# Kernel tuning notes

Measured on AMD Instinct MI355X. Metric: run time of the kernel, lower is better.

The kernel has to match this reference:

```python
import jax, jax.numpy as jnp
import numpy as np

DIM = 256
HEADS = 8
HD = DIM // HEADS  # 32
RPE_H = 512
STRIDE = 16
B, NQ = 4, 300
HH, WW = 64, 64
N = HH * WW


def setup_inputs() -> dict:
    key = jax.random.key(0)
    ks = jax.random.split(key, 24)

    def lin(k, fan_in, fan_out):
        return (jax.random.normal(k, (fan_in, fan_out), jnp.float32)
                / np.float32(np.sqrt(fan_in)))

    # boxes in absolute pixel coords (image is WW*STRIDE = 1024 px wide)
    rp_xy = jax.random.uniform(ks[0], (B, NQ, 1, 2), jnp.float32) * (WW * STRIDE)
    rp_wh = jax.random.uniform(ks[1], (B, NQ, 1, 2), jnp.float32) * 256.0 + 16.0
    reference_points = jnp.concatenate([rp_xy, rp_wh], axis=-1)  # [B,NQ,1,4]

    inp = {
        "query": jax.random.normal(ks[2], (B, NQ, DIM), jnp.float32),
        "reference_points": reference_points,
        "k_input_flatten": jax.random.normal(ks[3], (B, N, DIM), jnp.float32),
        "v_input_flatten": jax.random.normal(ks[4], (B, N, DIM), jnp.float32),
        "input_spatial_shapes": jnp.array([[HH, WW]], dtype=jnp.int32),
        "input_padding_mask": (jax.random.uniform(ks[5], (B, N)) < 0.1).astype(jnp.int32),
        # projections (stored as [in, out]; y = x @ W + b)
        "Wq": lin(ks[6], DIM, DIM), "bq": jnp.zeros((DIM,), jnp.float32),
        "Wk": lin(ks[7], DIM, DIM), "bk": jnp.zeros((DIM,), jnp.float32),
        "Wv": lin(ks[8], DIM, DIM), "bv": jnp.zeros((DIM,), jnp.float32),
        "Wp": lin(ks[9], DIM, DIM), "bp": jnp.zeros((DIM,), jnp.float32),
        # CPB MLP 1 (x-deltas): Linear(2,512)+ReLU+Linear(512,HEADS,no bias)
        "W1x": lin(ks[10], 2, RPE_H), "b1x": jnp.zeros((RPE_H,), jnp.float32),
        "W2x": lin(ks[11], RPE_H, HEADS),
        # CPB MLP 2 (y-deltas)
        "W1y": lin(ks[12], 2, RPE_H), "b1y": jnp.zeros((RPE_H,), jnp.float32),
        "W2y": lin(ks[13], RPE_H, HEADS),
    }
    return inp


def reference(query, reference_points, k_input_flatten, v_input_flatten,
              input_spatial_shapes, input_padding_mask,
              Wq, bq, Wk, bk, Wv, bv, Wp, bp,
              W1x, b1x, W2x, W1y, b1y, W2y):
    h = int(input_spatial_shapes[0, 0])
    w = int(input_spatial_shapes[0, 1])
    scale = HD ** -0.5

    # cxcywh -> (x1,y1,x2,y2)
    c, s = reference_points[..., :2], reference_points[..., 2:]
    ref_pts = jnp.concatenate([c - s / 2, c + s / 2], axis=-1)  # [B,NQ,1,4]

    pos_x = (jnp.arange(w, dtype=jnp.float32) + 0.5) * STRIDE  # [w]
    pos_y = (jnp.arange(h, dtype=jnp.float32) + 0.5) * STRIDE  # [h]
    delta_x = ref_pts[..., 0::2] - pos_x[None, None, :, None]  # [B,NQ,w,2]
    delta_y = ref_pts[..., 1::2] - pos_y[None, None, :, None]  # [B,NQ,h,2]

    rpe_x = jax.nn.relu(delta_x @ W1x + b1x) @ W2x  # [B,NQ,w,HEADS]
    rpe_y = jax.nn.relu(delta_y @ W1y + b1y) @ W2y  # [B,NQ,h,HEADS]
    rpe = rpe_x[:, :, None, :, :] + rpe_y[:, :, :, None, :]  # [B,NQ,h,w,H]

    Bq, Nq, C = query.shape
    rpe = rpe.reshape(Bq, Nq, h * w, HEADS).transpose(0, 3, 1, 2)  # [B,H,NQ,N]

    q = (query @ Wq + bq).reshape(Bq, Nq, HEADS, HD).transpose(0, 2, 1, 3) * scale
    k = (k_input_flatten @ Wk + bk).reshape(Bq, -1, HEADS, HD).transpose(0, 2, 1, 3)
    v = (v_input_flatten @ Wv + bv).reshape(Bq, -1, HEADS, HD).transpose(0, 2, 1, 3)

    attn = jnp.einsum('bhqd,bhkd->bhqk', q, k) + rpe
    attn = attn + input_padding_mask[:, None, None, :].astype(attn.dtype) * (-100.0)
    fi = jnp.finfo(attn.dtype)
    attn = jnp.clip(attn, fi.min, fi.max)
    attn = jax.nn.softmax(attn, axis=-1)

    x = jnp.einsum('bhqk,bhkd->bhqd', attn, v)
    x = x.transpose(0, 2, 1, 3).reshape(Bq, Nq, C)
    return x @ Wp + bp
```

## Files before the change

### kernel.cpp

```cpp
#include <hip/hip_runtime.h>
#include <math.h>

#define B_   4
#define NQ_  300
#define DIM_ 256
#define H_   8
#define HD_  32
#define N_   4096

typedef _Float16 f16;
typedef f16   f16x8 __attribute__((ext_vector_type(8)));
typedef f16   f16x4 __attribute__((ext_vector_type(4)));
typedef float f32x4 __attribute__((ext_vector_type(4)));

__global__ __launch_bounds__(256) void prep_wt(
    const float* __restrict__ Wq, const float* __restrict__ Wk,
    const float* __restrict__ Wv, const float* __restrict__ Wp,
    f16* __restrict__ WT, float qscale)
{
  __shared__ float t[64][65];
  const int z = blockIdx.z;
  const float* W = z == 0 ? Wq : z == 1 ? Wk : z == 2 ? Wv : Wp;
  const float s = z == 0 ? qscale : 1.0f;
  f16* O = WT + (size_t)z * 65536;
  const int k0 = blockIdx.y * 64, n0 = blockIdx.x * 64;
  const int r = threadIdx.x >> 2, c0 = (threadIdx.x & 3) * 16;
#pragma unroll
  for (int c = 0; c < 16; c += 4) {
    float4 v = *(const float4*)(W + (size_t)(k0 + r) * 256 + n0 + c0 + c);
    t[r][c0 + c] = v.x; t[r][c0 + c + 1] = v.y;
    t[r][c0 + c + 2] = v.z; t[r][c0 + c + 3] = v.w;
  }
  __syncthreads();
  f16* orow = O + (size_t)(n0 + r) * 256 + k0 + c0;
#pragma unroll
  for (int c = 0; c < 16; c += 4) {
    f16x4 p;
    p[0] = (f16)(t[c0 + c + 0][r] * s);
    p[1] = (f16)(t[c0 + c + 1][r] * s);
    p[2] = (f16)(t[c0 + c + 2][r] * s);
    p[3] = (f16)(t[c0 + c + 3][r] * s);
    *(f16x4*)(orow + c) = p;
  }
}

__device__ __forceinline__ void gemm_body(
    const void* __restrict__ Ain, const f16* __restrict__ WT,
    const float* __restrict__ bias, void* __restrict__ C,
    int M, float scale, int a_f16, int mode, int bm, int bn, int tid)
{
  __shared__ f16 As[64][40];
  __shared__ f16 Bs[64][40];
  const int lane = tid & 63;
  const int wv = tid >> 6;
  const int l15 = lane & 15, g = lane >> 4;
  const int arow = tid >> 2, akq = (tid & 3) * 8;

  f32x4 acc[4];
#pragma unroll
  for (int nt = 0; nt < 4; ++nt) acc[nt] = (f32x4){0.f, 0.f, 0.f, 0.f};

  for (int k0 = 0; k0 < 256; k0 += 32) {
    {
      const int gm = bm + arow;
      f16x8 av;
      if (gm < M) {
        if (a_f16 == 2) {
          const int bb2 = gm / NQ_, qq2 = gm % NQ_;
          const int kk = k0 + akq;
          av = *(const f16x8*)((const f16*)Ain +
              (((size_t)(bb2 * H_ + (kk >> 5)) * NQ_) + qq2) * 32 + (kk & 31));
        } else if (a_f16 == 1) {
          av = *(const f16x8*)((const f16*)Ain + (size_t)gm * 256 + k0 + akq);
        } else {
          const float* ap = (const float*)Ain + (size_t)gm * 256 + k0 + akq;
          float4 a0 = *(const float4*)ap;
          float4 a1 = *(const float4*)(ap + 4);
          av[0] = (f16)a0.x; av[1] = (f16)a0.y; av[2] = (f16)a0.z; av[3] = (f16)a0.w;
          av[4] = (f16)a1.x; av[5] = (f16)a1.y; av[6] = (f16)a1.z; av[7] = (f16)a1.w;
        }
      } else {
#pragma unroll
        for (int i = 0; i < 8; ++i) av[i] = (f16)0.f;
      }
      *(f16x8*)&As[arow][akq] = av;
      *(f16x8*)&Bs[arow][akq] =
          *(const f16x8*)(WT + (size_t)(bn + arow) * 256 + k0 + akq);
    }
    __syncthreads();
    const f16x8 af = *(const f16x8*)&As[wv * 16 + l15][g * 8];
#pragma unroll
    for (int nt = 0; nt < 4; ++nt) {
      const f16x8 bf = *(const f16x8*)&Bs[nt * 16 + l15][g * 8];
      acc[nt] = __builtin_amdgcn_mfma_f32_16x16x32_f16(af, bf, acc[nt], 0, 0, 0);
    }
    __syncthreads();
  }

#pragma unroll
  for (int nt = 0; nt < 4; ++nt) {
    const int n = bn + nt * 16 + l15;
    const float bv = bias[n] * scale;
    if (mode == 2) {
      const int m0 = bm + wv * 16 + g * 4;
      const int bb = m0 >> 12, nk = m0 & 4095;
      f16x4 pk;
#pragma unroll
      for (int r = 0; r < 4; ++r) pk[r] = (f16)(acc[nt][r] + bv);
      *(f16x4*)((f16*)C + (size_t)bb * (256 * 4096) + (size_t)n * 4096 + nk) = pk;
    } else {
#pragma unroll
      for (int r = 0; r < 4; ++r) {
        const int m = bm + wv * 16 + g * 4 + r;
        if (m >= M) continue;
        const float v = acc[nt][r] + bv;
        if (mode == 0)      ((float*)C)[(size_t)m * 256 + n] = v;
        else if (mode == 1) ((f16*)C)[(size_t)m * 256 + n] = (f16)v;
        else                ((f16*)C)[((((size_t)(m >> 12)) * H_ + (n >> 5)) * N_
                                       + (m & 4095)) * 32 + (n & 31)] = (f16)v;
      }
    }
  }
}

__global__ __launch_bounds__(256) void proj_qkv(
    const float* __restrict__ query, const float* __restrict__ kin,
    const float* __restrict__ vin, const f16* __restrict__ WT,
    const float* __restrict__ bq, const float* __restrict__ bk,
    const float* __restrict__ bv, f16* __restrict__ Qf,
    f16* __restrict__ Kf, f16* __restrict__ Vtf, float qscale)
{
  const int z = blockIdx.z;
  const int bm = blockIdx.y * 64, bn = blockIdx.x * 64;
  if (z == 0) {
    if (bm >= B_ * NQ_) return;
    gemm_body(query, WT, bq, Qf, B_ * NQ_, qscale, 0, 1, bm, bn, threadIdx.x);
  } else if (z == 1) {
    gemm_body(kin, WT + 65536, bk, Kf, B_ * N_, 1.0f, 0, 3, bm, bn, threadIdx.x);
  } else {
    gemm_body(vin, WT + 2 * 65536, bv, Vtf, B_ * N_, 1.0f, 0, 2, bm, bn, threadIdx.x);
  }
}

__global__ __launch_bounds__(256) void gemm_out(
    const f16* __restrict__ X, const f16* __restrict__ WT,
    const float* __restrict__ bp, float* __restrict__ out)
{
  gemm_body(X, WT + 3 * 65536, bp, out, B_ * NQ_, 1.0f, 2, 0,
            blockIdx.y * 64, blockIdx.x * 64, threadIdx.x);
}

__global__ __launch_bounds__(256) void rpe_kernel(
    const float* __restrict__ refpts,
    const float* __restrict__ W1x, const float* __restrict__ b1x, const float* __restrict__ W2x,
    const float* __restrict__ W1y, const float* __restrict__ b1y, const float* __restrict__ W2y,
    float* __restrict__ rpx, float* __restrict__ rpy)
{
  __shared__ float sRed[4][64][9];
  const int tid = threadIdx.x;
  const int lane = tid & 63;
  const int wv = __builtin_amdgcn_readfirstlane(tid >> 6);
  const int bq = blockIdx.x;
  const int axis = blockIdx.y;
  const float* W1 = axis ? W1y : W1x;
  const float* b1 = axis ? b1y : b1x;
  const float* W2 = axis ? W2y : W2x;
  float* out = axis ? rpy : rpx;

  const float c  = refpts[bq * 4 + axis];
  const float sz = refpts[bq * 4 + 2 + axis];
  const float pos = (lane + 0.5f) * 16.0f;
  const float d0 = c - 0.5f * sz - pos;
  const float d1 = c + 0.5f * sz - pos;
  float acc[8] = {};
  const int r0 = wv * 128;
#pragma unroll 4
  for (int i = 0; i < 128; ++i) {
    const int r = r0 + i;
    const float w10 = W1[r], w11 = W1[512 + r], bb = b1[r];
    const float hv = fmaxf(fmaf(d0, w10, fmaf(d1, w11, bb)), 0.0f);
    const float* w2r = W2 + r * 8;
#pragma unroll
    for (int hh = 0; hh < 8; ++hh) acc[hh] += hv * w2r[hh];
  }
#pragma unroll
  for (int hh = 0; hh < 8; ++hh) sRed[wv][lane][hh] = acc[hh];
  __syncthreads();
  for (int idx = tid; idx < 512; idx += 256) {
    const int hh = idx >> 6, jj = idx & 63;
    out[(size_t)bq * 512 + idx] =
        sRed[0][jj][hh] + sRed[1][jj][hh] + sRed[2][jj][hh] + sRed[3][jj][hh];
  }
}

__global__ __launch_bounds__(512, 4) void attn_mfma(
    const f16* __restrict__ Qf, const f16* __restrict__ Kf,
    const f16* __restrict__ Vtf, const float* __restrict__ rpx,
    const float* __restrict__ rpy, const int* __restrict__ mask,
    f16* __restrict__ X)
{
  __shared__ float smask[N_];
  __shared__ float srx[16][68];
  __shared__ float sry[16][68];
  __shared__ float mO[7][8][64];
  __shared__ float mlm[7][16];
  __shared__ float mll[7][16];

  const int tid = threadIdx.x;
  const int lane = tid & 63;
  const int kh = tid >> 6;
  const int bid = blockIdx.x;
  const int lg  = (bid & 7) * 80 + (bid >> 3);
  const int qg = lg % 20;
  const int h  = (lg / 20) % H_;
  const int b  = lg / (20 * H_);
  const int q0 = qg * 16;
  const float L2E = 1.44269504f;

  {
    const int4* mm4 = (const int4*)(mask + b * N_);
    for (int i = tid; i < N_ / 4; i += 512) {
      int4 mm = mm4[i];
      smask[4 * i + 0] = -100.f * L2E * (float)mm.x;
      smask[4 * i + 1] = -100.f * L2E * (float)mm.y;
      smask[4 * i + 2] = -100.f * L2E * (float)mm.z;
      smask[4 * i + 3] = -100.f * L2E * (float)mm.w;
    }
  }
  for (int i = tid; i < 1024; i += 512) {
    int qq = i >> 6, j = i & 63;
    int qg2 = q0 + qq; if (qg2 > NQ_ - 1) qg2 = NQ_ - 1;
    size_t base = (size_t)(b * NQ_ + qg2) * 512 + (size_t)h * 64 + j;
    srx[qq][j] = rpx[base] * L2E;
    sry[qq][j] = rpy[base] * L2E;
  }
  __syncthreads();

  const int l15 = lane & 15, g = lane >> 4;
  const int qrow0 = q0 + l15;
  const int qa = qrow0 > NQ_ - 1 ? NQ_ - 1 : qrow0;

  const f16x8 qf0 = *(const f16x8*)(Qf + (size_t)(b * NQ_ + qa) * 256 + h * 32 + g * 8);

  f32x4 O00 = {0.f,0.f,0.f,0.f}, O01 = {0.f,0.f,0.f,0.f};
  float lacc0 = 0.f;
  float mrun0 = -1e30f;
  const f16* kb  = Kf + (size_t)(b * H_ + h) * N_ * 32 + g * 8;
  const f16* v0p = Vtf + (size_t)(b * 256 + h * 32 + l15) * N_ + g * 4;
  const f16* v1p = v0p + (size_t)16 * N_;

  for (int sp = 0; sp < 8; ++sp) {
    const int kbase = kh * 512 + sp * 64;
    f16x8 kf[4];
    f16x4 va[4], vb[4];
#pragma unroll
    for (int cc = 0; cc < 4; ++cc) {
      kf[cc] = *(const f16x8*)(kb + (size_t)(kbase + cc * 16 + l15) * 32);
      va[cc] = *(const f16x4*)(v0p + kbase + cc * 16);
      vb[cc] = *(const f16x4*)(v1p + kbase + cc * 16);
    }
    f32x4 s0[4];
    float lm0 = -1e30f;
#pragma unroll
    for (int cc = 0; cc < 4; ++cc) {
      const int k0 = kbase + cc * 16;
      f32x4 S0 = __builtin_amdgcn_mfma_f32_16x16x32_f16(
          kf[cc], qf0, (f32x4){0.f,0.f,0.f,0.f}, 0, 0, 0);
      const float ry0 = sry[l15][k0 >> 6];
      const float4 rx0 = *(const float4*)&srx[l15][(k0 & 63) + g * 4];
      const float4 sm = *(const float4*)&smask[k0 + g * 4];
      s0[cc][0] = fmaf(S0[0], L2E, rx0.x + sm.x + ry0);
      s0[cc][1] = fmaf(S0[1], L2E, rx0.y + sm.y + ry0);
      s0[cc][2] = fmaf(S0[2], L2E, rx0.z + sm.z + ry0);
      s0[cc][3] = fmaf(S0[3], L2E, rx0.w + sm.w + ry0);
      lm0 = fmaxf(lm0, fmaxf(fmaxf(s0[cc][0], s0[cc][1]), fmaxf(s0[cc][2], s0[cc][3])));
    }
    lm0 = fmaxf(lm0, __shfl_xor(lm0, 16));
    lm0 = fmaxf(lm0, __shfl_xor(lm0, 32));
    const float mn0 = fmaxf(mrun0, lm0);
    const float f0 = exp2f(mrun0 - mn0);
    mrun0 = mn0;
    lacc0 *= f0;
#pragma unroll
    for (int r = 0; r < 4; ++r) { O00[r] *= f0; O01[r] *= f0; }
#pragma unroll
    for (int cc = 0; cc < 4; ++cc) {
      f16x4 pf0;
#pragma unroll
      for (int r = 0; r < 4; ++r) {
        const float p0 = exp2f(s0[cc][r] - mrun0);
        lacc0 += p0;
        pf0[r] = (f16)p0;
      }
      O00 = __builtin_amdgcn_mfma_f32_16x16x16f16(va[cc], pf0, O00, 0, 0, 0);
      O01 = __builtin_amdgcn_mfma_f32_16x16x16f16(vb[cc], pf0, O01, 0, 0, 0);
    }
  }

  lacc0 += __shfl_xor(lacc0, 16); lacc0 += __shfl_xor(lacc0, 32);

  if (kh > 0) {
#pragma unroll
    for (int r = 0; r < 4; ++r) {
      mO[kh - 1][r][lane]     = O00[r];
      mO[kh - 1][4 + r][lane] = O01[r];
    }
    if (lane < 16) {
      mlm[kh - 1][lane] = mrun0;
      mll[kh - 1][lane] = lacc0;
    }
  }
  __syncthreads();
  if (kh == 0) {
    float ms = mrun0;
#pragma unroll
    for (int w = 0; w < 7; ++w) ms = fmaxf(ms, mlm[w][l15]);
    const float fme = exp2f(mrun0 - ms);
    float lt = lacc0 * fme;
    float fw[7];
#pragma unroll
    for (int w = 0; w < 7; ++w) {
      fw[w] = exp2f(mlm[w][l15] - ms);
      lt += mll[w][l15] * fw[w];
    }
    const float rl = 1.0f / lt;
    if (qrow0 < NQ_) {
      f16* xr = X + ((size_t)(b * H_ + h) * NQ_ + qrow0) * 32;
      f16x4 p0, p1;
#pragma unroll
      for (int r = 0; r < 4; ++r) {
        float o0 = O00[r] * fme, o1 = O01[r] * fme;
#pragma unroll
        for (int w = 0; w < 7; ++w) {
          o0 += mO[w][r][lane] * fw[w];
          o1 += mO[w][4 + r][lane] * fw[w];
        }
        p0[r] = (f16)(o0 * rl);
        p1[r] = (f16)(o1 * rl);
      }
      *(f16x4*)(xr + g * 4) = p0;
      *(f16x4*)(xr + 16 + g * 4) = p1;
    }
  }
}

extern "C" void kernel_launch(void* const* d_in, const int* in_sizes, int n_in,
                              void* d_out, int out_size, void* d_ws, size_t ws_size,
                              hipStream_t stream)
{
  const float* query  = (const float*)d_in[0];
  const float* refpts = (const float*)d_in[1];
  const float* kin    = (const float*)d_in[2];
  const float* vin    = (const float*)d_in[3];
  const int*   mask   = (const int*)d_in[5];
  const float* Wq = (const float*)d_in[6];
  const float* bq = (const float*)d_in[7];
  const float* Wk = (const float*)d_in[8];
  const float* bk = (const float*)d_in[9];
  const float* Wv = (const float*)d_in[10];
  const float* bv = (const float*)d_in[11];
  const float* Wp = (const float*)d_in[12];
  const float* bp = (const float*)d_in[13];
  const float* W1x = (const float*)d_in[14];
  const float* b1x = (const float*)d_in[15];
  const float* W2x = (const float*)d_in[16];
  const float* W1y = (const float*)d_in[17];
  const float* b1y = (const float*)d_in[18];
  const float* W2y = (const float*)d_in[19];

  char* wsb = (char*)d_ws;
  f16*   Qf  = (f16*)(wsb);
  f16*   Kf  = (f16*)(wsb + 622592);
  f16*   Vtf = (f16*)(wsb + 9011200);
  float* rpx = (float*)(wsb + 17399808);
  float* rpy = (float*)(wsb + 19857408);
  f16*   X   = (f16*)(wsb + 22315008);
  f16*   WT  = (f16*)(wsb + 22937600);

  const float scale = 0.17677669529663687f;

  hipLaunchKernelGGL(prep_wt, dim3(4, 4, 4), dim3(256), 0, stream,
                     Wq, Wk, Wv, Wp, WT, scale);
  hipLaunchKernelGGL(rpe_kernel, dim3(B_ * NQ_, 2), dim3(256), 0, stream,
                     refpts, W1x, b1x, W2x, W1y, b1y, W2y, rpx, rpy);
  hipLaunchKernelGGL(proj_qkv, dim3(4, 256, 3), dim3(256), 0, stream,
                     query, kin, vin, WT, bq, bk, bv, Qf, Kf, Vtf, scale);
  hipLaunchKernelGGL(attn_mfma, dim3(B_ * H_ * 20), dim3(512), 0, stream,
                     Qf, Kf, Vtf, rpx, rpy, mask, X);
  hipLaunchKernelGGL(gemm_out, dim3(4, 19), dim3(256), 0, stream,
                     X, WT, bp, (float*)d_out);
}
```

Measured before the change: 231.3 us.

## Widen QKV projection tiles to full 256 output columns per block

Each proj_qkv block now computes a 64x256 output tile instead of 64x64. The A tile is loaded and fp32-to-fp16 converted once per block rather than four times, and the grid shrinks to 768 blocks. Block indices are remapped with an interleaving swizzle that spreads the Q, K and V work across dispatch order. The cost is 16 accumulator vectors per thread and a larger shared B buffer, which may lower occupancy. gemm_out also allocates the 4x larger Bs, and its runtime-bounded loops with nbt=1 may keep acc in scratch.

```diff
diff --git a/kernel.cpp b/kernel.cpp
--- a/kernel.cpp
+++ b/kernel.cpp
@@ -47,18 +47,20 @@
 __device__ __forceinline__ void gemm_body(
     const void* __restrict__ Ain, const f16* __restrict__ WT,
     const float* __restrict__ bias, void* __restrict__ C,
-    int M, float scale, int a_f16, int mode, int bm, int bn, int tid)
+    int M, float scale, int a_f16, int mode, int bm, int bn, int nbt, int tid)
 {
   __shared__ f16 As[64][40];
-  __shared__ f16 Bs[64][40];
+  __shared__ f16 Bs[4][64][40];
   const int lane = tid & 63;
   const int wv = tid >> 6;
   const int l15 = lane & 15, g = lane >> 4;
   const int arow = tid >> 2, akq = (tid & 3) * 8;
 
-  f32x4 acc[4];
-#pragma unroll
-  for (int nt = 0; nt < 4; ++nt) acc[nt] = (f32x4){0.f, 0.f, 0.f, 0.f};
+  f32x4 acc[4][4];
+#pragma unroll
+  for (int t = 0; t < 4; ++t)
+#pragma unroll
+    for (int nt = 0; nt < 4; ++nt) acc[t][nt] = (f32x4){0.f, 0.f, 0.f, 0.f};
 
   for (int k0 = 0; k0 < 256; k0 += 32) {
     {
@@ -84,40 +86,45 @@
         for (int i = 0; i < 8; ++i) av[i] = (f16)0.f;
       }
       *(f16x8*)&As[arow][akq] = av;
-      *(f16x8*)&Bs[arow][akq] =
-          *(const f16x8*)(WT + (size_t)(bn + arow) * 256 + k0 + akq);
+      for (int t = 0; t < nbt; ++t)
+        *(f16x8*)&Bs[t][arow][akq] =
+            *(const f16x8*)(WT + (size_t)(bn + t * 64 + arow) * 256 + k0 + akq);
     }
     __syncthreads();
     const f16x8 af = *(const f16x8*)&As[wv * 16 + l15][g * 8];
+    for (int t = 0; t < nbt; ++t) {
+#pragma unroll
+      for (int nt = 0; nt < 4; ++nt) {
+        const f16x8 bf = *(const f16x8*)&Bs[t][nt * 16 + l15][g * 8];
+        acc[t][nt] = __builtin_amdgcn_mfma_f32_16x16x32_f16(af, bf, acc[t][nt], 0, 0, 0);
+      }
+    }
+    __syncthreads();
+  }
+
+  for (int t = 0; t < nbt; ++t) {
 #pragma unroll
     for (int nt = 0; nt < 4; ++nt) {
-      const f16x8 bf = *(const f16x8*)&Bs[nt * 16 + l15][g * 8];
-      acc[nt] = __builtin_amdgcn_mfma_f32_16x16x32_f16(af, bf, acc[nt], 0, 0, 0);
-    }
-    __syncthreads();
-  }
-
-#pragma unroll
-  for (int nt = 0; nt < 4; ++nt) {
-    const int n = bn + nt * 16 + l15;
-    const float bv = bias[n] * scale;
-    if (mode == 2) {
-      const int m0 = bm + wv * 16 + g * 4;
-      const int bb = m0 >> 12, nk = m0 & 4095;
-      f16x4 pk;
-#pragma unroll
-      for (int r = 0; r < 4; ++r) pk[r] = (f16)(acc[nt][r] + bv);
-      *(f16x4*)((f16*)C + (size_t)bb * (256 * 4096) + (size_t)n * 4096 + nk) = pk;
-    } else {
-#pragma unroll
-      for (int r = 0; r < 4; ++r) {
-        const int m = bm + wv * 16 + g * 4 + r;
-        if (m >= M) continue;
-        const float v = acc[nt][r] + bv;
-        if (mode == 0)      ((float*)C)[(size_t)m * 256 + n] = v;
-        else if (mode == 1) ((f16*)C)[(size_t)m * 256 + n] = (f16)v;
-        else                ((f16*)C)[((((size_t)(m >> 12)) * H_ + (n >> 5)) * N_
-                                       + (m & 4095)) * 32 + (n & 31)] = (f16)v;
+      const int n = bn + t * 64 + nt * 16 + l15;
+      const float bv = bias[n] * scale;
+      if (mode == 2) {
+        const int m0 = bm + wv * 16 + g * 4;
+        const int bb = m0 >> 12, nk = m0 & 4095;
+        f16x4 pk;
+#pragma unroll
+        for (int r = 0; r < 4; ++r) pk[r] = (f16)(acc[t][nt][r] + bv);
+        *(f16x4*)((f16*)C + (size_t)bb * (256 * 4096) + (size_t)n * 4096 + nk) = pk;
+      } else {
+#pragma unroll
+        for (int r = 0; r < 4; ++r) {
+          const int m = bm + wv * 16 + g * 4 + r;
+          if (m >= M) continue;
+          const float v = acc[t][nt][r] + bv;
+          if (mode == 0)      ((float*)C)[(size_t)m * 256 + n] = v;
+          else if (mode == 1) ((f16*)C)[(size_t)m * 256 + n] = (f16)v;
+          else                ((f16*)C)[((((size_t)(m >> 12)) * H_ + (n >> 5)) * N_
+                                         + (m & 4095)) * 32 + (n & 31)] = (f16)v;
+        }
       }
     }
   }
@@ -130,15 +137,17 @@
     const float* __restrict__ bv, f16* __restrict__ Qf,
     f16* __restrict__ Kf, f16* __restrict__ Vtf, float qscale)
 {
-  const int z = blockIdx.z;
-  const int bm = blockIdx.y * 64, bn = blockIdx.x * 64;
+  const int bid = blockIdx.x;
+  const int lg  = (bid & 7) * 96 + (bid >> 3);
+  const int z   = lg >> 8;
+  const int bm  = (lg & 255) * 64;
   if (z == 0) {
     if (bm >= B_ * NQ_) return;
-    gemm_body(query, WT, bq, Qf, B_ * NQ_, qscale, 0, 1, bm, bn, threadIdx.x);
+    gemm_body(query, WT, bq, Qf, B_ * NQ_, qscale, 0, 1, bm, 0, 4, threadIdx.x);
   } else if (z == 1) {
-    gemm_body(kin, WT + 65536, bk, Kf, B_ * N_, 1.0f, 0, 3, bm, bn, threadIdx.x);
+    gemm_body(kin, WT + 65536, bk, Kf, B_ * N_, 1.0f, 0, 3, bm, 0, 4, threadIdx.x);
   } else {
-    gemm_body(vin, WT + 2 * 65536, bv, Vtf, B_ * N_, 1.0f, 0, 2, bm, bn, threadIdx.x);
+    gemm_body(vin, WT + 2 * 65536, bv, Vtf, B_ * N_, 1.0f, 0, 2, bm, 0, 4, threadIdx.x);
   }
 }
 
@@ -147,7 +156,7 @@
     const float* __restrict__ bp, float* __restrict__ out)
 {
   gemm_body(X, WT + 3 * 65536, bp, out, B_ * NQ_, 1.0f, 2, 0,
-            blockIdx.y * 64, blockIdx.x * 64, threadIdx.x);
+            blockIdx.y * 64, blockIdx.x * 64, 1, threadIdx.x);
 }
 
 __global__ __launch_bounds__(256) void rpe_kernel(
@@ -383,7 +392,7 @@
                      Wq, Wk, Wv, Wp, WT, scale);
   hipLaunchKernelGGL(rpe_kernel, dim3(B_ * NQ_, 2), dim3(256), 0, stream,
                      refpts, W1x, b1x, W2x, W1y, b1y, W2y, rpx, rpy);
-  hipLaunchKernelGGL(proj_qkv, dim3(4, 256, 3), dim3(256), 0, stream,
+  hipLaunchKernelGGL(proj_qkv, dim3(768), dim3(256), 0, stream,
                      query, kin, vin, WT, bq, bk, bv, Qf, Kf, Vtf, scale);
   hipLaunchKernelGGL(attn_mfma, dim3(B_ * H_ * 20), dim3(512), 0, stream,
                      Qf, Kf, Vtf, rpx, rpy, mask, X);
```

New measurement: 228.8 us. About the same (-1.1%).
